# Performance work log

Measured on AMD Instinct MI355X. Metric: run time of the kernel, lower is better.

Reference implementation:

```python
import jax, jax.numpy as jnp
import numpy as np

IN_C = 128
MID_C = 128
EPS = 1e-5


def layer_norm(x, g, b):
    mu = jnp.mean(x, axis=-1, keepdims=True)
    var = jnp.mean(jnp.square(x - mu), axis=-1, keepdims=True)
    return (x - mu) * jax.lax.rsqrt(var + EPS) * g + b


def setup_inputs() -> dict:
    key = jax.random.key(0)
    ks = jax.random.split(key, 16)
    B, N = 1, 384
    s_in = 1.0 / np.sqrt(IN_C)
    s_mid = 1.0 / np.sqrt(MID_C)
    return {
        "x2d": jax.random.normal(ks[0], (B, N, N, IN_C), dtype=jnp.float32),
        "n1_g": jnp.ones((IN_C,), jnp.float32),
        "n1_b": jnp.zeros((IN_C,), jnp.float32),
        "n2_g": jnp.ones((MID_C,), jnp.float32),
        "n2_b": jnp.zeros((MID_C,), jnp.float32),
        "w1i": jax.random.uniform(ks[1], (MID_C, IN_C), jnp.float32, -s_in, s_in),
        "b1i": jnp.zeros((MID_C,), jnp.float32),
        "w1j": jax.random.uniform(ks[2], (MID_C, IN_C), jnp.float32, -s_in, s_in),
        "b1j": jnp.zeros((MID_C,), jnp.float32),
        "w1i_s": jax.random.uniform(ks[3], (MID_C, IN_C), jnp.float32, -s_in, s_in),
        "b1i_s": jnp.zeros((MID_C,), jnp.float32),
        "w1j_s": jax.random.uniform(ks[4], (MID_C, IN_C), jnp.float32, -s_in, s_in),
        "b1j_s": jnp.zeros((MID_C,), jnp.float32),
        "w2": jax.random.uniform(ks[5], (IN_C, MID_C), jnp.float32, -s_mid, s_mid),
        "b2": jnp.zeros((IN_C,), jnp.float32),
        "w3": jax.random.uniform(ks[6], (IN_C, IN_C), jnp.float32, -s_in, s_in),
        "b3": jnp.zeros((IN_C,), jnp.float32),
    }


def reference(x2d, n1_g, n1_b, n2_g, n2_b, w1i, b1i, w1j, b1j,
              w1i_s, b1i_s, w1j_s, b1j_s, w2, b2, w3, b3):
    # x2d: [B, N, N, C]
    x = layer_norm(x2d, n1_g, n1_b)
    i = (x @ w1i.T + b1i) * jax.nn.sigmoid(x @ w1i_s.T + b1i_s)  # [B,N,N,mid]
    j = (x @ w1j.T + b1j) * jax.nn.sigmoid(x @ w1j_s.T + b1j_s)  # [B,N,N,mid]
    out = jnp.einsum('bikc,bjkc->bijc', i, j)                    # contract over k
    out = layer_norm(out, n2_g, n2_b)
    out = out @ w2.T + b2
    out = out * jax.nn.sigmoid(x @ w3.T + b3)
    return out
```

## Files before the change

### kernel.cpp

```cpp
#include <hip/hip_runtime.h>

#define NN 384
#define CC 128
#define NPOS (NN * NN)

typedef short bf8_t __attribute__((ext_vector_type(8)));
typedef float f32x4_t __attribute__((ext_vector_type(4)));

#define MFMA16(a, b, c) __builtin_amdgcn_mfma_f32_16x16x32_bf16((a), (b), (c), 0, 0, 0)

__device__ __forceinline__ unsigned short f2bf(float f) {
  unsigned int u = __builtin_bit_cast(unsigned int, f);
  u += 0x7fffu + ((u >> 16) & 1u);
  return (unsigned short)(u >> 16);
}
__device__ __forceinline__ float bf2f(unsigned short s) {
  return __builtin_bit_cast(float, ((unsigned int)s) << 16);
}
__device__ __forceinline__ float sigm(float x) {
  float e = __builtin_amdgcn_exp2f(x * -1.44269504f);
  return __builtin_amdgcn_rcpf(1.0f + e);
}

__global__ __launch_bounds__(256) void kW(const float* __restrict__ a,
                                          const float* __restrict__ b,
                                          const float* __restrict__ c,
                                          const float* __restrict__ d,
                                          const float* __restrict__ e,
                                          const float* __restrict__ f,
                                          unsigned short* __restrict__ o) {
  int idx = (blockIdx.x * 256 + threadIdx.x) * 4;
  const float* s = f;
  if (idx < 16384) s = a;
  else if (idx < 32768) s = b;
  else if (idx < 49152) s = c;
  else if (idx < 65536) s = d;
  else if (idx < 81920) s = e;
  int off = idx & 16383;
  float4 v = *(const float4*)(s + off);
  o[idx + 0] = f2bf(v.x);
  o[idx + 1] = f2bf(v.y);
  o[idx + 2] = f2bf(v.z);
  o[idx + 3] = f2bf(v.w);
}

__global__ __launch_bounds__(256) void kLN(const float* __restrict__ x,
                                           const float* __restrict__ n1g,
                                           const float* __restrict__ n1b,
                                           unsigned short* __restrict__ x_ln) {
  int t = threadIdx.x;
  int pos = blockIdx.x * 128 + (t >> 1);
  int half = t & 1;
  const float* xr = x + (size_t)pos * CC + half * 64;
  float v[64];
  float s = 0.f;
#pragma unroll
  for (int a = 0; a < 16; ++a) {
    float4 f4 = ((const float4*)xr)[a];
    v[4 * a + 0] = f4.x; v[4 * a + 1] = f4.y;
    v[4 * a + 2] = f4.z; v[4 * a + 3] = f4.w;
    s += f4.x + f4.y + f4.z + f4.w;
  }
  s += __shfl_xor(s, 1);
  float mu = s * (1.0f / CC);
  float vs = 0.f;
#pragma unroll
  for (int a = 0; a < 64; ++a) { float d = v[a] - mu; vs += d * d; }
  vs += __shfl_xor(vs, 1);
  float rs = rsqrtf(vs * (1.0f / CC) + 1e-5f);
  unsigned short* dst = x_ln + (size_t)pos * CC + half * 64;
#pragma unroll
  for (int a8 = 0; a8 < 8; ++a8) {
    union { bf8_t v8; unsigned short e[8]; } u;
#pragma unroll
    for (int e = 0; e < 8; ++e) {
      int c = half * 64 + a8 * 8 + e;
      u.e[e] = f2bf((v[a8 * 8 + e] - mu) * rs * n1g[c] + n1b[c]);
    }
    *(bf8_t*)(dst + a8 * 8) = u.v8;
  }
}

__global__ __launch_bounds__(256, 2) void kP(
    const unsigned short* __restrict__ x_ln, const unsigned short* __restrict__ wcat,
    const float* __restrict__ b1i, const float* __restrict__ b1is,
    const float* __restrict__ b1j, const float* __restrict__ b1js,
    const float* __restrict__ b3v, unsigned short* __restrict__ i_s,
    unsigned short* __restrict__ j_s, unsigned short* __restrict__ g3) {
  __shared__ __align__(16) unsigned short lds[16640];
  float* bl = (float*)(lds + 16384);

  int b = blockIdx.x;
  int xcd = b & 7, m = b >> 3;
  int tl = m / 6, job = m % 6;
  int pt = xcd * 144 + tl;
  int p = job >> 1, h = job & 1;
  int p0 = pt * 128;
  int t = threadIdx.x, lane = t & 63, wave = t >> 6;
  int lr = lane & 15, lh = lane >> 4;

  bf8_t xf[2][4];
#pragma unroll
  for (int nt = 0; nt < 2; ++nt)
#pragma unroll
    for (int kk = 0; kk < 4; ++kk)
      xf[nt][kk] = *(const bf8_t*)(x_ln + (size_t)(p0 + wave * 32 + nt * 16 + lr) * CC +
                                   kk * 32 + lh * 8);

  int mV = p * 2;
  const unsigned short* Wv = wcat + (size_t)mV * CC * CC + h * 64 * CC;
#pragma unroll
  for (int it = 0; it < 4; ++it) {
    int u = it * 256 + t;
    int row = u >> 4, sl = u & 15;
    int slg = sl ^ (row & 7);
    __builtin_amdgcn_global_load_lds(
        (const __attribute__((address_space(1))) unsigned int*)(Wv + row * CC + slg * 8),
        (__attribute__((address_space(3))) unsigned int*)(lds + u * 8), 16, 0, 0);
  }
  if (p < 2) {
    const unsigned short* Wg = wcat + (size_t)(mV + 1) * CC * CC + h * 64 * CC;
#pragma unroll
    for (int it = 0; it < 4; ++it) {
      int u = it * 256 + t;
      int row = u >> 4, sl = u & 15;
      int slg = sl ^ (row & 7);
      __builtin_amdgcn_global_load_lds(
          (const __attribute__((address_space(1))) unsigned int*)(Wg + row * CC + slg * 8),
          (__attribute__((address_space(3))) unsigned int*)(lds + 8192 + u * 8), 16, 0, 0);
    }
  }
  {
    const float* bvp = (p == 0) ? b1i : (p == 1) ? b1j : b3v;
    if (t < 16) ((float4*)bl)[t] = ((const float4*)(bvp + h * 64))[t];
    if (p < 2 && t >= 16 && t < 32) {
      const float* bgp = (p == 0) ? b1is : b1js;
      ((float4*)bl)[t] = ((const float4*)(bgp + h * 64))[t - 16];
    }
  }
  __syncthreads();

  float blv[16], blg[16];
  if (p < 2) {
#pragma unroll
    for (int ct = 0; ct < 4; ++ct)
#pragma unroll
      for (int r = 0; r < 4; ++r) {
        blv[ct * 4 + r] = bl[ct * 16 + lh * 4 + r];
        blg[ct * 4 + r] = bl[64 + ct * 16 + lh * 4 + r];
      }
  } else {
#pragma unroll
    for (int ct = 0; ct < 4; ++ct) blv[ct] = bl[ct * 16 + lr];
  }

  f32x4_t z4 = {0.f, 0.f, 0.f, 0.f};
  f32x4_t accV[2][4], accG[2][4];
#pragma unroll
  for (int nt = 0; nt < 2; ++nt)
#pragma unroll
    for (int ct = 0; ct < 4; ++ct) { accV[nt][ct] = z4; accG[nt][ct] = z4; }
#pragma unroll
  for (int ct = 0; ct < 4; ++ct)
#pragma unroll
    for (int kk = 0; kk < 4; ++kk) {
      int rv = ct * 16 + lr;
      int slot = (kk * 4 + lh) ^ (rv & 7);
      bf8_t wv = *(const bf8_t*)&lds[rv * 128 + slot * 8];
      if (p < 2) {
        bf8_t wg = *(const bf8_t*)&lds[8192 + rv * 128 + slot * 8];
#pragma unroll
        for (int nt = 0; nt < 2; ++nt) {
          accV[nt][ct] = MFMA16(wv, xf[nt][kk], accV[nt][ct]);
          accG[nt][ct] = MFMA16(wg, xf[nt][kk], accG[nt][ct]);
        }
      } else {
#pragma unroll
        for (int nt = 0; nt < 2; ++nt)
          accV[nt][ct] = MFMA16(xf[nt][kk], wv, accV[nt][ct]);
      }
    }
  __syncthreads();

  if (p < 2) {
#pragma unroll
    for (int nt = 0; nt < 2; ++nt)
#pragma unroll
      for (int ct = 0; ct < 4; ++ct)
#pragma unroll
        for (int r = 0; r < 4; ++r) {
          int cl = ct * 16 + lh * 4 + r;
          int pos = wave * 32 + nt * 16 + lr;
          float o = (accV[nt][ct][r] + blv[ct * 4 + r]) *
                    sigm(accG[nt][ct][r] + blg[ct * 4 + r]);
          int sw = ((ct * 4 + lh) & 7) << 4;
          lds[cl * 128 + (pos ^ sw)] = f2bf(o);
        }
    __syncthreads();
    unsigned short* dstm = p ? j_s : i_s;
#pragma unroll
    for (int it = 0; it < 4; ++it) {
      int u = it * 256 + t;
      int cl = u >> 4, ch = u & 15;
      int s = (cl >> 2) & 7;
      bf8_t v = *(const bf8_t*)&lds[cl * 128 + ((ch ^ (s << 1)) * 8)];
      *(bf8_t*)(dstm + (size_t)(h * 64 + cl) * NPOS + p0 + ch * 8) = v;
    }
  } else {
#pragma unroll
    for (int nt = 0; nt < 2; ++nt)
#pragma unroll
      for (int ct = 0; ct < 4; ++ct)
#pragma unroll
        for (int r = 0; r < 4; ++r) {
          int pos = wave * 32 + nt * 16 + lh * 4 + r;
          int cl = ct * 16 + lr;
          float o = sigm(accV[nt][ct][r] + blv[ct]);
          int slot = (cl >> 3) ^ (pos & 7);
          lds[pos * 64 + slot * 8 + (cl & 7)] = f2bf(o);
        }
    __syncthreads();
#pragma unroll
    for (int it = 0; it < 4; ++it) {
      int u = it * 256 + t;
      int pos = u >> 3, ch = u & 7;
      int slot = ch ^ (pos & 7);
      bf8_t v = *(const bf8_t*)&lds[pos * 64 + slot * 8];
      *(bf8_t*)(g3 + (size_t)(p0 + pos) * CC + h * 64 + ch * 8) = v;
    }
  }
}

__global__ __launch_bounds__(256) void kB(const unsigned short* __restrict__ i_s,
                                          const unsigned short* __restrict__ j_s,
                                          unsigned short* __restrict__ out_pre) {
  __shared__ unsigned short At[128][32];
  __shared__ unsigned short Bt[128][32];
  int b = blockIdx.x;
  int logical = (b & 7) * 144 + (b >> 3);
  int c = logical / 9;
  int tt = logical % 9;
  int i0 = (tt / 3) * 128, j0 = (tt % 3) * 128;
  const unsigned short* Ab = i_s + ((size_t)c * NN + i0) * NN;
  const unsigned short* Bb = j_s + ((size_t)c * NN + j0) * NN;
  int t = threadIdx.x, lane = t & 63, wave = t >> 6;
  int wi = (wave >> 1) * 64, wj = (wave & 1) * 64;
  int lr = lane & 15, lh = lane >> 4;
  int rsub = lane >> 2;
  int ksub = (lane & 3) * 8;

  f32x4_t z4 = {0.f, 0.f, 0.f, 0.f};
  f32x4_t acc[4][4];
#pragma unroll
  for (int mt = 0; mt < 4; ++mt)
#pragma unroll
    for (int nt = 0; nt < 4; ++nt) acc[mt][nt] = z4;

  for (int k0 = 0; k0 < NN; k0 += 32) {
#pragma unroll
    for (int half = 0; half < 2; ++half) {
      int r = half * 64 + wave * 16;
      __builtin_amdgcn_global_load_lds(
          (const __attribute__((address_space(1))) unsigned int*)(Ab + (size_t)(r + rsub) * NN + k0 + ksub),
          (__attribute__((address_space(3))) unsigned int*)&At[r][0], 16, 0, 0);
      __builtin_amdgcn_global_load_lds(
          (const __attribute__((address_space(1))) unsigned int*)(Bb + (size_t)(r + rsub) * NN + k0 + ksub),
          (__attribute__((address_space(3))) unsigned int*)&Bt[r][0], 16, 0, 0);
    }
    __syncthreads();
    bf8_t af2[4], bf2[4];
#pragma unroll
    for (int mt = 0; mt < 4; ++mt) af2[mt] = *(const bf8_t*)&At[wi + mt * 16 + lr][lh * 8];
#pragma unroll
    for (int nt = 0; nt < 4; ++nt) bf2[nt] = *(const bf8_t*)&Bt[wj + nt * 16 + lr][lh * 8];
#pragma unroll
    for (int mt = 0; mt < 4; ++mt)
#pragma unroll
      for (int nt = 0; nt < 4; ++nt) acc[mt][nt] = MFMA16(af2[mt], bf2[nt], acc[mt][nt]);
    __syncthreads();
  }
  unsigned short* orow = out_pre + ((size_t)c * NN + (i0 + wi)) * NN + (j0 + wj);
#pragma unroll
  for (int mt = 0; mt < 4; ++mt)
#pragma unroll
    for (int nt = 0; nt < 4; ++nt)
#pragma unroll
      for (int r = 0; r < 4; ++r)
        orow[(size_t)(mt * 16 + lh * 4 + r) * NN + nt * 16 + lr] = f2bf(acc[mt][nt][r]);
}

__global__ __launch_bounds__(256, 2) void kC(const unsigned short* __restrict__ out_pre,
                                             const float* __restrict__ n2g,
                                             const float* __restrict__ n2b,
                                             const unsigned short* __restrict__ w2bf,
                                             const float* __restrict__ b2,
                                             const unsigned short* __restrict__ g3,
                                             float* __restrict__ out) {
  __shared__ __align__(16) unsigned short ldsu[17408];
  int b = blockIdx.x;
  int ii = b / 3, j0 = (b % 3) * 128;
  int t = threadIdx.x, lane = t & 63, wave = t >> 6;

#pragma unroll
  for (int it = 0; it < 8; ++it) {
    int u = it * 256 + t;
    int c = u >> 4, jg = u & 15;
    __builtin_amdgcn_global_load_lds(
        (const __attribute__((address_space(1))) unsigned int*)(out_pre + ((size_t)c * NN + ii) * NN + j0 + jg * 8),
        (__attribute__((address_space(3))) unsigned int*)(ldsu + u * 8), 16, 0, 0);
  }
  __syncthreads();

  {
    int pos = t >> 1, half = t & 1;
    float v[64];
    float s = 0.f;
#pragma unroll
    for (int a = 0; a < 64; ++a) { v[a] = bf2f(ldsu[(half * 64 + a) * 128 + pos]); s += v[a]; }
    s += __shfl_xor(s, 1);
    float mu = s * (1.0f / CC);
    float vs = 0.f;
#pragma unroll
    for (int a = 0; a < 64; ++a) { float d = v[a] - mu; vs += d * d; }
    vs += __shfl_xor(vs, 1);
    float rs = rsqrtf(vs * (1.0f / CC) + 1e-5f);
    union { bf8_t v8[8]; unsigned short e[64]; } u;
#pragma unroll
    for (int a = 0; a < 64; ++a) {
      int c = half * 64 + a;
      u.e[a] = f2bf((v[a] - mu) * rs * n2g[c] + n2b[c]);
    }
    __syncthreads();
#pragma unroll
    for (int a8 = 0; a8 < 8; ++a8)
      *(bf8_t*)&ldsu[pos * 136 + half * 64 + a8 * 8] = u.v8[a8];
  }
  __syncthreads();

  int lr = lane & 15, lh = lane >> 4;
  bf8_t af2[2][4];
#pragma unroll
  for (int mt = 0; mt < 2; ++mt)
#pragma unroll
    for (int kk = 0; kk < 4; ++kk)
      af2[mt][kk] = *(const bf8_t*)&ldsu[(wave * 32 + mt * 16 + lr) * 136 + kk * 32 + lh * 8];
  f32x4_t z4 = {0.f, 0.f, 0.f, 0.f};
  f32x4_t acc[2][8];
#pragma unroll
  for (int mt = 0; mt < 2; ++mt)
#pragma unroll
    for (int nt = 0; nt < 8; ++nt) acc[mt][nt] = z4;
#pragma unroll
  for (int nt = 0; nt < 8; ++nt) {
#pragma unroll
    for (int kk = 0; kk < 4; ++kk) {
      bf8_t bw = *(const bf8_t*)(w2bf + (size_t)(nt * 16 + lr) * CC + kk * 32 + lh * 8);
#pragma unroll
      for (int mt = 0; mt < 2; ++mt) acc[mt][nt] = MFMA16(af2[mt][kk], bw, acc[mt][nt]);
    }
  }
#pragma unroll
  for (int mt = 0; mt < 2; ++mt)
#pragma unroll
    for (int nt = 0; nt < 8; ++nt)
#pragma unroll
      for (int r = 0; r < 4; ++r) {
        int posl = wave * 32 + mt * 16 + lh * 4 + r;
        int c = nt * 16 + lr;
        size_t p = (size_t)ii * NN + j0 + posl;
        float y = acc[mt][nt][r] + b2[c];
        out[p * CC + c] = y * bf2f(g3[p * CC + c]);
      }
}

extern "C" void kernel_launch(void* const* d_in, const int* in_sizes, int n_in,
                              void* d_out, int out_size, void* d_ws, size_t ws_size,
                              hipStream_t stream) {
  (void)in_sizes; (void)n_in; (void)out_size; (void)ws_size;
  const float* x2d  = (const float*)d_in[0];
  const float* n1g  = (const float*)d_in[1];
  const float* n1b  = (const float*)d_in[2];
  const float* n2g  = (const float*)d_in[3];
  const float* n2b  = (const float*)d_in[4];
  const float* w1i  = (const float*)d_in[5];
  const float* b1i  = (const float*)d_in[6];
  const float* w1j  = (const float*)d_in[7];
  const float* b1j  = (const float*)d_in[8];
  const float* w1is = (const float*)d_in[9];
  const float* b1is = (const float*)d_in[10];
  const float* w1js = (const float*)d_in[11];
  const float* b1js = (const float*)d_in[12];
  const float* w2   = (const float*)d_in[13];
  const float* b2   = (const float*)d_in[14];
  const float* w3   = (const float*)d_in[15];
  const float* b3   = (const float*)d_in[16];

  char* ws = (char*)d_ws;
  unsigned short* wcat = (unsigned short*)ws;
  size_t TELEMS = (size_t)CC * NN * NN;
  unsigned short* i_s  = (unsigned short*)(ws + 262144);
  unsigned short* j_s  = i_s + TELEMS;
  unsigned short* g3   = j_s + TELEMS;
  unsigned short* x_ln = g3 + TELEMS;
  unsigned short* out_pre = x_ln;
  float* outp = (float*)d_out;

  kW<<<96, 256, 0, stream>>>(w1i, w1is, w1j, w1js, w3, w2, wcat);
  kLN<<<1152, 256, 0, stream>>>(x2d, n1g, n1b, x_ln);
  kP<<<6912, 256, 0, stream>>>(x_ln, wcat, b1i, b1is, b1j, b1js, b3, i_s, j_s, g3);
  kB<<<1152, 256, 0, stream>>>(i_s, j_s, out_pre);
  kC<<<1152, 256, 0, stream>>>(out_pre, n2g, n2b, wcat + 5 * CC * CC, b2, g3, outp);
}
```

Measured before the change: 178.0 us.

## Shrink kP tiles to 64 positions x 32 channels for higher occupancy

```diff
diff --git a/kernel.cpp b/kernel.cpp
--- a/kernel.cpp
+++ b/kernel.cpp
@@ -81,36 +81,32 @@
   }
 }
 
-__global__ __launch_bounds__(256, 2) void kP(
+__global__ __launch_bounds__(256, 8) void kP(
     const unsigned short* __restrict__ x_ln, const unsigned short* __restrict__ wcat,
     const float* __restrict__ b1i, const float* __restrict__ b1is,
     const float* __restrict__ b1j, const float* __restrict__ b1js,
     const float* __restrict__ b3v, unsigned short* __restrict__ i_s,
     unsigned short* __restrict__ j_s, unsigned short* __restrict__ g3) {
-  __shared__ __align__(16) unsigned short lds[16640];
-  float* bl = (float*)(lds + 16384);
+  __shared__ __align__(16) unsigned short lds[8448];
+  float* bl = (float*)(lds + 8192);
 
   int b = blockIdx.x;
   int xcd = b & 7, m = b >> 3;
-  int tl = m / 6, job = m % 6;
-  int pt = xcd * 144 + tl;
-  int p = job >> 1, h = job & 1;
-  int p0 = pt * 128;
+  int ht = m / 12, job = m % 12;
+  int p = job >> 2, q = job & 3;
+  int c0 = q * 32;
+  int p0 = (xcd * 288 + ht) * 64;
   int t = threadIdx.x, lane = t & 63, wave = t >> 6;
   int lr = lane & 15, lh = lane >> 4;
 
-  bf8_t xf[2][4];
-#pragma unroll
-  for (int nt = 0; nt < 2; ++nt)
-#pragma unroll
-    for (int kk = 0; kk < 4; ++kk)
-      xf[nt][kk] = *(const bf8_t*)(x_ln + (size_t)(p0 + wave * 32 + nt * 16 + lr) * CC +
-                                   kk * 32 + lh * 8);
-
-  int mV = p * 2;
-  const unsigned short* Wv = wcat + (size_t)mV * CC * CC + h * 64 * CC;
-#pragma unroll
-  for (int it = 0; it < 4; ++it) {
+  bf8_t xf[4];
+#pragma unroll
+  for (int kk = 0; kk < 4; ++kk)
+    xf[kk] = *(const bf8_t*)(x_ln + (size_t)(p0 + wave * 16 + lr) * CC + kk * 32 + lh * 8);
+
+  const unsigned short* Wv = wcat + (size_t)(p < 2 ? p * 2 : 4) * CC * CC + c0 * CC;
+#pragma unroll
+  for (int it = 0; it < 2; ++it) {
     int u = it * 256 + t;
     int row = u >> 4, sl = u & 15;
     int slg = sl ^ (row & 7);
@@ -119,115 +115,83 @@
         (__attribute__((address_space(3))) unsigned int*)(lds + u * 8), 16, 0, 0);
   }
   if (p < 2) {
-    const unsigned short* Wg = wcat + (size_t)(mV + 1) * CC * CC + h * 64 * CC;
-#pragma unroll
-    for (int it = 0; it < 4; ++it) {
+    const unsigned short* Wg = Wv + CC * CC;
+#pragma unroll
+    for (int it = 0; it < 2; ++it) {
       int u = it * 256 + t;
       int row = u >> 4, sl = u & 15;
       int slg = sl ^ (row & 7);
       __builtin_amdgcn_global_load_lds(
           (const __attribute__((address_space(1))) unsigned int*)(Wg + row * CC + slg * 8),
-          (__attribute__((address_space(3))) unsigned int*)(lds + 8192 + u * 8), 16, 0, 0);
+          (__attribute__((address_space(3))) unsigned int*)(lds + 4096 + u * 8), 16, 0, 0);
     }
   }
   {
     const float* bvp = (p == 0) ? b1i : (p == 1) ? b1j : b3v;
-    if (t < 16) ((float4*)bl)[t] = ((const float4*)(bvp + h * 64))[t];
-    if (p < 2 && t >= 16 && t < 32) {
+    if (t < 8) ((float4*)bl)[t] = ((const float4*)(bvp + c0))[t];
+    if (p < 2 && t >= 8 && t < 16) {
       const float* bgp = (p == 0) ? b1is : b1js;
-      ((float4*)bl)[t] = ((const float4*)(bgp + h * 64))[t - 16];
+      ((float4*)bl)[t] = ((const float4*)(bgp + c0))[t - 8];
     }
   }
   __syncthreads();
 
-  float blv[16], blg[16];
+  f32x4_t z4 = {0.f, 0.f, 0.f, 0.f};
+  f32x4_t accV[2] = {z4, z4}, accG[2] = {z4, z4};
   if (p < 2) {
 #pragma unroll
-    for (int ct = 0; ct < 4; ++ct)
+    for (int ct = 0; ct < 2; ++ct)
+#pragma unroll
+      for (int kk = 0; kk < 4; ++kk) {
+        int rv = ct * 16 + lr;
+        int slot = (kk * 4 + lh) ^ (rv & 7);
+        bf8_t wv = *(const bf8_t*)&lds[rv * 128 + slot * 8];
+        bf8_t wg = *(const bf8_t*)&lds[4096 + rv * 128 + slot * 8];
+        accV[ct] = MFMA16(wv, xf[kk], accV[ct]);
+        accG[ct] = MFMA16(wg, xf[kk], accG[ct]);
+      }
+  } else {
+#pragma unroll
+    for (int ct = 0; ct < 2; ++ct)
+#pragma unroll
+      for (int kk = 0; kk < 4; ++kk) {
+        int rv = ct * 16 + lr;
+        int slot = (kk * 4 + lh) ^ (rv & 7);
+        bf8_t wv = *(const bf8_t*)&lds[rv * 128 + slot * 8];
+        accV[ct] = MFMA16(xf[kk], wv, accV[ct]);
+      }
+  }
+  __syncthreads();
+
+  if (p < 2) {
+#pragma unroll
+    for (int ct = 0; ct < 2; ++ct)
 #pragma unroll
       for (int r = 0; r < 4; ++r) {
-        blv[ct * 4 + r] = bl[ct * 16 + lh * 4 + r];
-        blg[ct * 4 + r] = bl[64 + ct * 16 + lh * 4 + r];
-      }
+        int cl = ct * 16 + lh * 4 + r;
+        int pos = wave * 16 + lr;
+        float o = (accV[ct][r] + bl[cl]) * sigm(accG[ct][r] + bl[32 + cl]);
+        lds[cl * 72 + pos] = f2bf(o);
+      }
+    __syncthreads();
+    unsigned short* dstm = p ? j_s : i_s;
+    int cl = t >> 3, ch = t & 7;
+    bf8_t v = *(const bf8_t*)&lds[cl * 72 + ch * 8];
+    *(bf8_t*)(dstm + (size_t)(c0 + cl) * NPOS + p0 + ch * 8) = v;
   } else {
 #pragma unroll
-    for (int ct = 0; ct < 4; ++ct) blv[ct] = bl[ct * 16 + lr];
-  }
-
-  f32x4_t z4 = {0.f, 0.f, 0.f, 0.f};
-  f32x4_t accV[2][4], accG[2][4];
-#pragma unroll
-  for (int nt = 0; nt < 2; ++nt)
-#pragma unroll
-    for (int ct = 0; ct < 4; ++ct) { accV[nt][ct] = z4; accG[nt][ct] = z4; }
-#pragma unroll
-  for (int ct = 0; ct < 4; ++ct)
-#pragma unroll
-    for (int kk = 0; kk < 4; ++kk) {
-      int rv = ct * 16 + lr;
-      int slot = (kk * 4 + lh) ^ (rv & 7);
-      bf8_t wv = *(const bf8_t*)&lds[rv * 128 + slot * 8];
-      if (p < 2) {
-        bf8_t wg = *(const bf8_t*)&lds[8192 + rv * 128 + slot * 8];
-#pragma unroll
-        for (int nt = 0; nt < 2; ++nt) {
-          accV[nt][ct] = MFMA16(wv, xf[nt][kk], accV[nt][ct]);
-          accG[nt][ct] = MFMA16(wg, xf[nt][kk], accG[nt][ct]);
-        }
-      } else {
-#pragma unroll
-        for (int nt = 0; nt < 2; ++nt)
-          accV[nt][ct] = MFMA16(xf[nt][kk], wv, accV[nt][ct]);
-      }
-    }
-  __syncthreads();
-
-  if (p < 2) {
-#pragma unroll
-    for (int nt = 0; nt < 2; ++nt)
-#pragma unroll
-      for (int ct = 0; ct < 4; ++ct)
-#pragma unroll
-        for (int r = 0; r < 4; ++r) {
-          int cl = ct * 16 + lh * 4 + r;
-          int pos = wave * 32 + nt * 16 + lr;
-          float o = (accV[nt][ct][r] + blv[ct * 4 + r]) *
-                    sigm(accG[nt][ct][r] + blg[ct * 4 + r]);
-          int sw = ((ct * 4 + lh) & 7) << 4;
-          lds[cl * 128 + (pos ^ sw)] = f2bf(o);
-        }
-    __syncthreads();
-    unsigned short* dstm = p ? j_s : i_s;
-#pragma unroll
-    for (int it = 0; it < 4; ++it) {
-      int u = it * 256 + t;
-      int cl = u >> 4, ch = u & 15;
-      int s = (cl >> 2) & 7;
-      bf8_t v = *(const bf8_t*)&lds[cl * 128 + ((ch ^ (s << 1)) * 8)];
-      *(bf8_t*)(dstm + (size_t)(h * 64 + cl) * NPOS + p0 + ch * 8) = v;
-    }
-  } else {
-#pragma unroll
-    for (int nt = 0; nt < 2; ++nt)
-#pragma unroll
-      for (int ct = 0; ct < 4; ++ct)
-#pragma unroll
-        for (int r = 0; r < 4; ++r) {
-          int pos = wave * 32 + nt * 16 + lh * 4 + r;
-          int cl = ct * 16 + lr;
-          float o = sigm(accV[nt][ct][r] + blv[ct]);
-          int slot = (cl >> 3) ^ (pos & 7);
-          lds[pos * 64 + slot * 8 + (cl & 7)] = f2bf(o);
-        }
-    __syncthreads();
-#pragma unroll
-    for (int it = 0; it < 4; ++it) {
-      int u = it * 256 + t;
-      int pos = u >> 3, ch = u & 7;
-      int slot = ch ^ (pos & 7);
-      bf8_t v = *(const bf8_t*)&lds[pos * 64 + slot * 8];
-      *(bf8_t*)(g3 + (size_t)(p0 + pos) * CC + h * 64 + ch * 8) = v;
-    }
+    for (int ct = 0; ct < 2; ++ct)
+#pragma unroll
+      for (int r = 0; r < 4; ++r) {
+        int pos = wave * 16 + lh * 4 + r;
+        int cl = ct * 16 + lr;
+        float o = sigm(accV[ct][r] + bl[cl]);
+        lds[pos * 40 + cl] = f2bf(o);
+      }
+    __syncthreads();
+    int posl = t >> 2, ch = t & 3;
+    bf8_t v = *(const bf8_t*)&lds[posl * 40 + ch * 8];
+    *(bf8_t*)(g3 + (size_t)(p0 + posl) * CC + c0 + ch * 8) = v;
   }
 }
 
@@ -407,7 +371,7 @@
 
   kW<<<96, 256, 0, stream>>>(w1i, w1is, w1j, w1js, w3, w2, wcat);
   kLN<<<1152, 256, 0, stream>>>(x2d, n1g, n1b, x_ln);
-  kP<<<6912, 256, 0, stream>>>(x_ln, wcat, b1i, b1is, b1j, b1js, b3, i_s, j_s, g3);
+  kP<<<27648, 256, 0, stream>>>(x_ln, wcat, b1i, b1is, b1j, b1js, b3, i_s, j_s, g3);
   kB<<<1152, 256, 0, stream>>>(i_s, j_s, out_pre);
   kC<<<1152, 256, 0, stream>>>(out_pre, n2g, n2b, wcat + 5 * CC * CC, b2, g3, outp);
 }
```

Measured after the change: 191.1 us. 7.4% more time.

## Fuse the sigmoid(x@w3) gate projection into the final kernel, dropping the g3 buffer

Applied to the files above, without the earlier changes.

```diff
diff --git a/kernel.cpp b/kernel.cpp
--- a/kernel.cpp
+++ b/kernel.cpp
@@ -85,14 +85,13 @@
     const unsigned short* __restrict__ x_ln, const unsigned short* __restrict__ wcat,
     const float* __restrict__ b1i, const float* __restrict__ b1is,
     const float* __restrict__ b1j, const float* __restrict__ b1js,
-    const float* __restrict__ b3v, unsigned short* __restrict__ i_s,
-    unsigned short* __restrict__ j_s, unsigned short* __restrict__ g3) {
+    unsigned short* __restrict__ i_s, unsigned short* __restrict__ j_s) {
   __shared__ __align__(16) unsigned short lds[16640];
   float* bl = (float*)(lds + 16384);
 
   int b = blockIdx.x;
   int xcd = b & 7, m = b >> 3;
-  int tl = m / 6, job = m % 6;
+  int tl = m / 4, job = m % 4;
   int pt = xcd * 144 + tl;
   int p = job >> 1, h = job & 1;
   int p0 = pt * 128;
@@ -107,8 +106,7 @@
       xf[nt][kk] = *(const bf8_t*)(x_ln + (size_t)(p0 + wave * 32 + nt * 16 + lr) * CC +
                                    kk * 32 + lh * 8);
 
-  int mV = p * 2;
-  const unsigned short* Wv = wcat + (size_t)mV * CC * CC + h * 64 * CC;
+  const unsigned short* Wv = wcat + (size_t)(p * 2) * CC * CC + h * 64 * CC;
 #pragma unroll
   for (int it = 0; it < 4; ++it) {
     int u = it * 256 + t;
@@ -118,8 +116,8 @@
         (const __attribute__((address_space(1))) unsigned int*)(Wv + row * CC + slg * 8),
         (__attribute__((address_space(3))) unsigned int*)(lds + u * 8), 16, 0, 0);
   }
-  if (p < 2) {
-    const unsigned short* Wg = wcat + (size_t)(mV + 1) * CC * CC + h * 64 * CC;
+  {
+    const unsigned short* Wg = Wv + CC * CC;
 #pragma unroll
     for (int it = 0; it < 4; ++it) {
       int u = it * 256 + t;
@@ -131,28 +129,23 @@
     }
   }
   {
-    const float* bvp = (p == 0) ? b1i : (p == 1) ? b1j : b3v;
+    const float* bvp = p ? b1j : b1i;
     if (t < 16) ((float4*)bl)[t] = ((const float4*)(bvp + h * 64))[t];
-    if (p < 2 && t >= 16 && t < 32) {
-      const float* bgp = (p == 0) ? b1is : b1js;
+    if (t >= 16 && t < 32) {
+      const float* bgp = p ? b1js : b1is;
       ((float4*)bl)[t] = ((const float4*)(bgp + h * 64))[t - 16];
     }
   }
   __syncthreads();
 
   float blv[16], blg[16];
-  if (p < 2) {
-#pragma unroll
-    for (int ct = 0; ct < 4; ++ct)
-#pragma unroll
-      for (int r = 0; r < 4; ++r) {
-        blv[ct * 4 + r] = bl[ct * 16 + lh * 4 + r];
-        blg[ct * 4 + r] = bl[64 + ct * 16 + lh * 4 + r];
-      }
-  } else {
-#pragma unroll
-    for (int ct = 0; ct < 4; ++ct) blv[ct] = bl[ct * 16 + lr];
-  }
+#pragma unroll
+  for (int ct = 0; ct < 4; ++ct)
+#pragma unroll
+    for (int r = 0; r < 4; ++r) {
+      blv[ct * 4 + r] = bl[ct * 16 + lh * 4 + r];
+      blg[ct * 4 + r] = bl[64 + ct * 16 + lh * 4 + r];
+    }
 
   f32x4_t z4 = {0.f, 0.f, 0.f, 0.f};
   f32x4_t accV[2][4], accG[2][4];
@@ -167,67 +160,37 @@
       int rv = ct * 16 + lr;
       int slot = (kk * 4 + lh) ^ (rv & 7);
       bf8_t wv = *(const bf8_t*)&lds[rv * 128 + slot * 8];
-      if (p < 2) {
-        bf8_t wg = *(const bf8_t*)&lds[8192 + rv * 128 + slot * 8];
-#pragma unroll
-        for (int nt = 0; nt < 2; ++nt) {
-          accV[nt][ct] = MFMA16(wv, xf[nt][kk], accV[nt][ct]);
-          accG[nt][ct] = MFMA16(wg, xf[nt][kk], accG[nt][ct]);
-        }
-      } else {
-#pragma unroll
-        for (int nt = 0; nt < 2; ++nt)
-          accV[nt][ct] = MFMA16(xf[nt][kk], wv, accV[nt][ct]);
+      bf8_t wg = *(const bf8_t*)&lds[8192 + rv * 128 + slot * 8];
+#pragma unroll
+      for (int nt = 0; nt < 2; ++nt) {
+        accV[nt][ct] = MFMA16(wv, xf[nt][kk], accV[nt][ct]);
+        accG[nt][ct] = MFMA16(wg, xf[nt][kk], accG[nt][ct]);
       }
     }
   __syncthreads();
 
-  if (p < 2) {
-#pragma unroll
-    for (int nt = 0; nt < 2; ++nt)
-#pragma unroll
-      for (int ct = 0; ct < 4; ++ct)
-#pragma unroll
-        for (int r = 0; r < 4; ++r) {
-          int cl = ct * 16 + lh * 4 + r;
-          int pos = wave * 32 + nt * 16 + lr;
-          float o = (accV[nt][ct][r] + blv[ct * 4 + r]) *
-                    sigm(accG[nt][ct][r] + blg[ct * 4 + r]);
-          int sw = ((ct * 4 + lh) & 7) << 4;
-          lds[cl * 128 + (pos ^ sw)] = f2bf(o);
-        }
-    __syncthreads();
-    unsigned short* dstm = p ? j_s : i_s;
-#pragma unroll
-    for (int it = 0; it < 4; ++it) {
-      int u = it * 256 + t;
-      int cl = u >> 4, ch = u & 15;
-      int s = (cl >> 2) & 7;
-      bf8_t v = *(const bf8_t*)&lds[cl * 128 + ((ch ^ (s << 1)) * 8)];
-      *(bf8_t*)(dstm + (size_t)(h * 64 + cl) * NPOS + p0 + ch * 8) = v;
-    }
-  } else {
-#pragma unroll
-    for (int nt = 0; nt < 2; ++nt)
-#pragma unroll
-      for (int ct = 0; ct < 4; ++ct)
-#pragma unroll
-        for (int r = 0; r < 4; ++r) {
-          int pos = wave * 32 + nt * 16 + lh * 4 + r;
-          int cl = ct * 16 + lr;
-          float o = sigm(accV[nt][ct][r] + blv[ct]);
-          int slot = (cl >> 3) ^ (pos & 7);
-          lds[pos * 64 + slot * 8 + (cl & 7)] = f2bf(o);
-        }
-    __syncthreads();
-#pragma unroll
-    for (int it = 0; it < 4; ++it) {
-      int u = it * 256 + t;
-      int pos = u >> 3, ch = u & 7;
-      int slot = ch ^ (pos & 7);
-      bf8_t v = *(const bf8_t*)&lds[pos * 64 + slot * 8];
-      *(bf8_t*)(g3 + (size_t)(p0 + pos) * CC + h * 64 + ch * 8) = v;
-    }
+#pragma unroll
+  for (int nt = 0; nt < 2; ++nt)
+#pragma unroll
+    for (int ct = 0; ct < 4; ++ct)
+#pragma unroll
+      for (int r = 0; r < 4; ++r) {
+        int cl = ct * 16 + lh * 4 + r;
+        int pos = wave * 32 + nt * 16 + lr;
+        float o = (accV[nt][ct][r] + blv[ct * 4 + r]) *
+                  sigm(accG[nt][ct][r] + blg[ct * 4 + r]);
+        int sw = ((ct * 4 + lh) & 7) << 4;
+        lds[cl * 128 + (pos ^ sw)] = f2bf(o);
+      }
+  __syncthreads();
+  unsigned short* dstm = p ? j_s : i_s;
+#pragma unroll
+  for (int it = 0; it < 4; ++it) {
+    int u = it * 256 + t;
+    int cl = u >> 4, ch = u & 15;
+    int s = (cl >> 2) & 7;
+    bf8_t v = *(const bf8_t*)&lds[cl * 128 + ((ch ^ (s << 1)) * 8)];
+    *(bf8_t*)(dstm + (size_t)(h * 64 + cl) * NPOS + p0 + ch * 8) = v;
   }
 }
 
@@ -292,14 +255,24 @@
 __global__ __launch_bounds__(256, 2) void kC(const unsigned short* __restrict__ out_pre,
                                              const float* __restrict__ n2g,
                                              const float* __restrict__ n2b,
-                                             const unsigned short* __restrict__ w2bf,
+                                             const unsigned short* __restrict__ wcat,
                                              const float* __restrict__ b2,
-                                             const unsigned short* __restrict__ g3,
+                                             const float* __restrict__ b3v,
+                                             const unsigned short* __restrict__ x_ln,
                                              float* __restrict__ out) {
   __shared__ __align__(16) unsigned short ldsu[17408];
   int b = blockIdx.x;
   int ii = b / 3, j0 = (b % 3) * 128;
   int t = threadIdx.x, lane = t & 63, wave = t >> 6;
+  int lr = lane & 15, lh = lane >> 4;
+
+  bf8_t xf3[2][4];
+#pragma unroll
+  for (int mt = 0; mt < 2; ++mt)
+#pragma unroll
+    for (int kk = 0; kk < 4; ++kk)
+      xf3[mt][kk] = *(const bf8_t*)(x_ln + (size_t)(ii * NN + j0 + wave * 32 + mt * 16 + lr) * CC +
+                                    kk * 32 + lh * 8);
 
 #pragma unroll
   for (int it = 0; it < 8; ++it) {
@@ -309,6 +282,41 @@
         (const __attribute__((address_space(1))) unsigned int*)(out_pre + ((size_t)c * NN + ii) * NN + j0 + jg * 8),
         (__attribute__((address_space(3))) unsigned int*)(ldsu + u * 8), 16, 0, 0);
   }
+
+  const unsigned short* w3bf = wcat + (size_t)4 * CC * CC;
+  f32x4_t z4 = {0.f, 0.f, 0.f, 0.f};
+  unsigned int g3p[2][8][2];
+#pragma unroll
+  for (int qd = 0; qd < 2; ++qd) {
+    f32x4_t acc3[2][4];
+#pragma unroll
+    for (int mt = 0; mt < 2; ++mt)
+#pragma unroll
+      for (int nq = 0; nq < 4; ++nq) acc3[mt][nq] = z4;
+#pragma unroll
+    for (int nq = 0; nq < 4; ++nq) {
+      int nt = qd * 4 + nq;
+#pragma unroll
+      for (int kk = 0; kk < 4; ++kk) {
+        bf8_t bw = *(const bf8_t*)(w3bf + (size_t)(nt * 16 + lr) * CC + kk * 32 + lh * 8);
+#pragma unroll
+        for (int mt = 0; mt < 2; ++mt) acc3[mt][nq] = MFMA16(xf3[mt][kk], bw, acc3[mt][nq]);
+      }
+    }
+#pragma unroll
+    for (int nq = 0; nq < 4; ++nq) {
+      int nt = qd * 4 + nq;
+      float b3c = b3v[nt * 16 + lr];
+#pragma unroll
+      for (int mt = 0; mt < 2; ++mt)
+#pragma unroll
+        for (int rp = 0; rp < 2; ++rp) {
+          float o0 = sigm(acc3[mt][nq][rp * 2 + 0] + b3c);
+          float o1 = sigm(acc3[mt][nq][rp * 2 + 1] + b3c);
+          g3p[mt][nt][rp] = (unsigned int)f2bf(o0) | ((unsigned int)f2bf(o1) << 16);
+        }
+    }
+  }
   __syncthreads();
 
   {
@@ -337,14 +345,13 @@
   }
   __syncthreads();
 
-  int lr = lane & 15, lh = lane >> 4;
+  const unsigned short* w2bf = wcat + (size_t)5 * CC * CC;
   bf8_t af2[2][4];
 #pragma unroll
   for (int mt = 0; mt < 2; ++mt)
 #pragma unroll
     for (int kk = 0; kk < 4; ++kk)
       af2[mt][kk] = *(const bf8_t*)&ldsu[(wave * 32 + mt * 16 + lr) * 136 + kk * 32 + lh * 8];
-  f32x4_t z4 = {0.f, 0.f, 0.f, 0.f};
   f32x4_t acc[2][8];
 #pragma unroll
   for (int mt = 0; mt < 2; ++mt)
@@ -369,7 +376,8 @@
         int c = nt * 16 + lr;
         size_t p = (size_t)ii * NN + j0 + posl;
         float y = acc[mt][nt][r] + b2[c];
-        out[p * CC + c] = y * bf2f(g3[p * CC + c]);
+        float g = bf2f((unsigned short)(g3p[mt][nt][r >> 1] >> ((r & 1) * 16)));
+        out[p * CC + c] = y * g;
       }
 }
 
@@ -398,16 +406,15 @@
   char* ws = (char*)d_ws;
   unsigned short* wcat = (unsigned short*)ws;
   size_t TELEMS = (size_t)CC * NN * NN;
-  unsigned short* i_s  = (unsigned short*)(ws + 262144);
-  unsigned short* j_s  = i_s + TELEMS;
-  unsigned short* g3   = j_s + TELEMS;
-  unsigned short* x_ln = g3 + TELEMS;
-  unsigned short* out_pre = x_ln;
+  unsigned short* i_s     = (unsigned short*)(ws + 262144);
+  unsigned short* j_s     = i_s + TELEMS;
+  unsigned short* x_ln    = j_s + TELEMS;
+  unsigned short* out_pre = x_ln + TELEMS;
   float* outp = (float*)d_out;
 
   kW<<<96, 256, 0, stream>>>(w1i, w1is, w1j, w1js, w3, w2, wcat);
   kLN<<<1152, 256, 0, stream>>>(x2d, n1g, n1b, x_ln);
-  kP<<<6912, 256, 0, stream>>>(x_ln, wcat, b1i, b1is, b1j, b1js, b3, i_s, j_s, g3);
+  kP<<<4608, 256, 0, stream>>>(x_ln, wcat, b1i, b1is, b1j, b1js, i_s, j_s);
   kB<<<1152, 256, 0, stream>>>(i_s, j_s, out_pre);
-  kC<<<1152, 256, 0, stream>>>(out_pre, n2g, n2b, wcat + 5 * CC * CC, b2, g3, outp);
-}
+  kC<<<1152, 256, 0, stream>>>(out_pre, n2g, n2b, wcat, b2, b3, x_ln, outp);
+}
```

After: 180.6 us. Within noise of the previous version (+1.5%).

## Make projection blocks persistent over four position tiles with prefetched activations

Applied to the files above, without the earlier changes.

```diff
diff --git a/kernel.cpp b/kernel.cpp
--- a/kernel.cpp
+++ b/kernel.cpp
@@ -3,6 +3,7 @@
 #define NN 384
 #define CC 128
 #define NPOS (NN * NN)
+#define TPB 4
 
 typedef short bf8_t __attribute__((ext_vector_type(8)));
 typedef float f32x4_t __attribute__((ext_vector_type(4)));
@@ -87,28 +88,18 @@
     const float* __restrict__ b1j, const float* __restrict__ b1js,
     const float* __restrict__ b3v, unsigned short* __restrict__ i_s,
     unsigned short* __restrict__ j_s, unsigned short* __restrict__ g3) {
-  __shared__ __align__(16) unsigned short lds[16640];
-  float* bl = (float*)(lds + 16384);
+  __shared__ __align__(16) unsigned short lds[24832];
+  unsigned short* gt = lds + 16384;
+  float* bl = (float*)(lds + 24576);
 
   int b = blockIdx.x;
   int xcd = b & 7, m = b >> 3;
-  int tl = m / 6, job = m % 6;
-  int pt = xcd * 144 + tl;
+  int group = m / 6, job = m % 6;
   int p = job >> 1, h = job & 1;
-  int p0 = pt * 128;
   int t = threadIdx.x, lane = t & 63, wave = t >> 6;
   int lr = lane & 15, lh = lane >> 4;
 
-  bf8_t xf[2][4];
-#pragma unroll
-  for (int nt = 0; nt < 2; ++nt)
-#pragma unroll
-    for (int kk = 0; kk < 4; ++kk)
-      xf[nt][kk] = *(const bf8_t*)(x_ln + (size_t)(p0 + wave * 32 + nt * 16 + lr) * CC +
-                                   kk * 32 + lh * 8);
-
-  int mV = p * 2;
-  const unsigned short* Wv = wcat + (size_t)mV * CC * CC + h * 64 * CC;
+  const unsigned short* Wv = wcat + (size_t)(p < 2 ? p * 2 : 4) * CC * CC + h * 64 * CC;
 #pragma unroll
   for (int it = 0; it < 4; ++it) {
     int u = it * 256 + t;
@@ -119,7 +110,7 @@
         (__attribute__((address_space(3))) unsigned int*)(lds + u * 8), 16, 0, 0);
   }
   if (p < 2) {
-    const unsigned short* Wg = wcat + (size_t)(mV + 1) * CC * CC + h * 64 * CC;
+    const unsigned short* Wg = Wv + CC * CC;
 #pragma unroll
     for (int it = 0; it < 4; ++it) {
       int u = it * 256 + t;
@@ -130,104 +121,118 @@
           (__attribute__((address_space(3))) unsigned int*)(lds + 8192 + u * 8), 16, 0, 0);
     }
   }
-  {
-    const float* bvp = (p == 0) ? b1i : (p == 1) ? b1j : b3v;
+  if (p < 2) {
+    const float* bvp = p ? b1j : b1i;
+    const float* bgp = p ? b1js : b1is;
     if (t < 16) ((float4*)bl)[t] = ((const float4*)(bvp + h * 64))[t];
-    if (p < 2 && t >= 16 && t < 32) {
-      const float* bgp = (p == 0) ? b1is : b1js;
-      ((float4*)bl)[t] = ((const float4*)(bgp + h * 64))[t - 16];
-    }
-  }
+    else if (t < 32) ((float4*)bl)[t] = ((const float4*)(bgp + h * 64))[t - 16];
+  } else {
+    if (t < 16) ((float4*)bl)[t] = ((const float4*)(b3v + h * 64))[t];
+  }
+
+  int pt0 = xcd * 144 + group * TPB;
+  bf8_t xfA[2][4], xfB[2][4];
+#define LOADXF(xf, tt)                                                               \
+  {                                                                                  \
+    int p0l = (pt0 + (tt)) * 128;                                                    \
+    _Pragma("unroll") for (int nt = 0; nt < 2; ++nt)                                 \
+        _Pragma("unroll") for (int kk = 0; kk < 4; ++kk)                             \
+            xf[nt][kk] = *(const bf8_t*)(x_ln +                                      \
+                                         (size_t)(p0l + wave * 32 + nt * 16 + lr) *  \
+                                             CC + kk * 32 + lh * 8);                 \
+  }
+  LOADXF(xfA, 0);
   __syncthreads();
 
-  float blv[16], blg[16];
-  if (p < 2) {
-#pragma unroll
-    for (int ct = 0; ct < 4; ++ct)
-#pragma unroll
-      for (int r = 0; r < 4; ++r) {
-        blv[ct * 4 + r] = bl[ct * 16 + lh * 4 + r];
-        blg[ct * 4 + r] = bl[64 + ct * 16 + lh * 4 + r];
+  f32x4_t z4 = {0.f, 0.f, 0.f, 0.f};
+#pragma unroll
+  for (int tt = 0; tt < TPB; ++tt) {
+    int p0 = (pt0 + tt) * 128;
+    bf8_t(&xfc)[2][4] = (tt & 1) ? xfB : xfA;
+    bf8_t(&xfn)[2][4] = (tt & 1) ? xfA : xfB;
+    if (tt + 1 < TPB) LOADXF(xfn, tt + 1);
+
+    f32x4_t accV[2][4], accG[2][4];
+#pragma unroll
+    for (int nt = 0; nt < 2; ++nt)
+#pragma unroll
+      for (int ct = 0; ct < 4; ++ct) { accV[nt][ct] = z4; accG[nt][ct] = z4; }
+    if (p < 2) {
+#pragma unroll
+      for (int ct = 0; ct < 4; ++ct)
+#pragma unroll
+        for (int kk = 0; kk < 4; ++kk) {
+          int rv = ct * 16 + lr;
+          int slot = (kk * 4 + lh) ^ (rv & 7);
+          bf8_t wv = *(const bf8_t*)&lds[rv * 128 + slot * 8];
+          bf8_t wg = *(const bf8_t*)&lds[8192 + rv * 128 + slot * 8];
+#pragma unroll
+          for (int nt = 0; nt < 2; ++nt) {
+            accV[nt][ct] = MFMA16(wv, xfc[nt][kk], accV[nt][ct]);
+            accG[nt][ct] = MFMA16(wg, xfc[nt][kk], accG[nt][ct]);
+          }
+        }
+    } else {
+#pragma unroll
+      for (int ct = 0; ct < 4; ++ct)
+#pragma unroll
+        for (int kk = 0; kk < 4; ++kk) {
+          int rv = ct * 16 + lr;
+          int slot = (kk * 4 + lh) ^ (rv & 7);
+          bf8_t wv = *(const bf8_t*)&lds[rv * 128 + slot * 8];
+#pragma unroll
+          for (int nt = 0; nt < 2; ++nt)
+            accV[nt][ct] = MFMA16(xfc[nt][kk], wv, accV[nt][ct]);
+        }
+    }
+
+    if (p < 2) {
+#pragma unroll
+      for (int nt = 0; nt < 2; ++nt)
+#pragma unroll
+        for (int ct = 0; ct < 4; ++ct)
+#pragma unroll
+          for (int r = 0; r < 4; ++r) {
+            int cl = ct * 16 + lh * 4 + r;
+            int pos = wave * 32 + nt * 16 + lr;
+            float o = (accV[nt][ct][r] + bl[cl]) * sigm(accG[nt][ct][r] + bl[64 + cl]);
+            int sw = ((ct * 4 + lh) & 7) << 4;
+            gt[cl * 128 + (pos ^ sw)] = f2bf(o);
+          }
+      __syncthreads();
+      unsigned short* dstm = p ? j_s : i_s;
+#pragma unroll
+      for (int it = 0; it < 4; ++it) {
+        int u = it * 256 + t;
+        int cl = u >> 4, ch = u & 15;
+        int s = (cl >> 2) & 7;
+        bf8_t v = *(const bf8_t*)&gt[cl * 128 + ((ch ^ (s << 1)) * 8)];
+        *(bf8_t*)(dstm + (size_t)(h * 64 + cl) * NPOS + p0 + ch * 8) = v;
       }
-  } else {
-#pragma unroll
-    for (int ct = 0; ct < 4; ++ct) blv[ct] = bl[ct * 16 + lr];
-  }
-
-  f32x4_t z4 = {0.f, 0.f, 0.f, 0.f};
-  f32x4_t accV[2][4], accG[2][4];
-#pragma unroll
-  for (int nt = 0; nt < 2; ++nt)
-#pragma unroll
-    for (int ct = 0; ct < 4; ++ct) { accV[nt][ct] = z4; accG[nt][ct] = z4; }
-#pragma unroll
-  for (int ct = 0; ct < 4; ++ct)
-#pragma unroll
-    for (int kk = 0; kk < 4; ++kk) {
-      int rv = ct * 16 + lr;
-      int slot = (kk * 4 + lh) ^ (rv & 7);
-      bf8_t wv = *(const bf8_t*)&lds[rv * 128 + slot * 8];
-      if (p < 2) {
-        bf8_t wg = *(const bf8_t*)&lds[8192 + rv * 128 + slot * 8];
-#pragma unroll
-        for (int nt = 0; nt < 2; ++nt) {
-          accV[nt][ct] = MFMA16(wv, xf[nt][kk], accV[nt][ct]);
-          accG[nt][ct] = MFMA16(wg, xf[nt][kk], accG[nt][ct]);
-        }
-      } else {
-#pragma unroll
-        for (int nt = 0; nt < 2; ++nt)
-          accV[nt][ct] = MFMA16(xf[nt][kk], wv, accV[nt][ct]);
+    } else {
+#pragma unroll
+      for (int nt = 0; nt < 2; ++nt)
+#pragma unroll
+        for (int ct = 0; ct < 4; ++ct)
+#pragma unroll
+          for (int r = 0; r < 4; ++r) {
+            int pos = wave * 32 + nt * 16 + lh * 4 + r;
+            int cl = ct * 16 + lr;
+            float o = sigm(accV[nt][ct][r] + bl[cl]);
+            int slot = (cl >> 3) ^ (pos & 7);
+            gt[pos * 64 + slot * 8 + (cl & 7)] = f2bf(o);
+          }
+      __syncthreads();
+#pragma unroll
+      for (int it = 0; it < 4; ++it) {
+        int u = it * 256 + t;
+        int pos = u >> 3, ch = u & 7;
+        int slot = ch ^ (pos & 7);
+        bf8_t v = *(const bf8_t*)&gt[pos * 64 + slot * 8];
+        *(bf8_t*)(g3 + (size_t)(p0 + pos) * CC + h * 64 + ch * 8) = v;
       }
     }
-  __syncthreads();
-
-  if (p < 2) {
-#pragma unroll
-    for (int nt = 0; nt < 2; ++nt)
-#pragma unroll
-      for (int ct = 0; ct < 4; ++ct)
-#pragma unroll
-        for (int r = 0; r < 4; ++r) {
-          int cl = ct * 16 + lh * 4 + r;
-          int pos = wave * 32 + nt * 16 + lr;
-          float o = (accV[nt][ct][r] + blv[ct * 4 + r]) *
-                    sigm(accG[nt][ct][r] + blg[ct * 4 + r]);
-          int sw = ((ct * 4 + lh) & 7) << 4;
-          lds[cl * 128 + (pos ^ sw)] = f2bf(o);
-        }
     __syncthreads();
-    unsigned short* dstm = p ? j_s : i_s;
-#pragma unroll
-    for (int it = 0; it < 4; ++it) {
-      int u = it * 256 + t;
-      int cl = u >> 4, ch = u & 15;
-      int s = (cl >> 2) & 7;
-      bf8_t v = *(const bf8_t*)&lds[cl * 128 + ((ch ^ (s << 1)) * 8)];
-      *(bf8_t*)(dstm + (size_t)(h * 64 + cl) * NPOS + p0 + ch * 8) = v;
-    }
-  } else {
-#pragma unroll
-    for (int nt = 0; nt < 2; ++nt)
-#pragma unroll
-      for (int ct = 0; ct < 4; ++ct)
-#pragma unroll
-        for (int r = 0; r < 4; ++r) {
-          int pos = wave * 32 + nt * 16 + lh * 4 + r;
-          int cl = ct * 16 + lr;
-          float o = sigm(accV[nt][ct][r] + blv[ct]);
-          int slot = (cl >> 3) ^ (pos & 7);
-          lds[pos * 64 + slot * 8 + (cl & 7)] = f2bf(o);
-        }
-    __syncthreads();
-#pragma unroll
-    for (int it = 0; it < 4; ++it) {
-      int u = it * 256 + t;
-      int pos = u >> 3, ch = u & 7;
-      int slot = ch ^ (pos & 7);
-      bf8_t v = *(const bf8_t*)&lds[pos * 64 + slot * 8];
-      *(bf8_t*)(g3 + (size_t)(p0 + pos) * CC + h * 64 + ch * 8) = v;
-    }
   }
 }
 
@@ -407,7 +412,7 @@
 
   kW<<<96, 256, 0, stream>>>(w1i, w1is, w1j, w1js, w3, w2, wcat);
   kLN<<<1152, 256, 0, stream>>>(x2d, n1g, n1b, x_ln);
-  kP<<<6912, 256, 0, stream>>>(x_ln, wcat, b1i, b1is, b1j, b1js, b3, i_s, j_s, g3);
+  kP<<<1728, 256, 0, stream>>>(x_ln, wcat, b1i, b1is, b1j, b1js, b3, i_s, j_s, g3);
   kB<<<1152, 256, 0, stream>>>(i_s, j_s, out_pre);
   kC<<<1152, 256, 0, stream>>>(out_pre, n2g, n2b, wcat + 5 * CC * CC, b2, g3, outp);
 }
```

Measured after the change: 176.6 us. No clear change (-0.8%).
